# Kernel optimization log

Hardware: AMD Instinct MI355X
Metric: run time of the kernel (lower is better)

Reference implementation:

```python
import jax, jax.numpy as jnp
import numpy as np

NUM_HEADS = 16

def setup_inputs() -> dict:
    key = jax.random.key(0)
    ks = jax.random.split(key, 5)
    B, N, C = 2, 2048, 1024
    x = jax.random.normal(ks[0], (B, N, C), dtype=jnp.float32)
    s_in = 1.0 / np.sqrt(C)
    Wq = jax.random.normal(ks[1], (C, 2 * C), dtype=jnp.float32) * s_in
    Wk = jax.random.normal(ks[2], (C, 2 * C), dtype=jnp.float32) * s_in
    Wv = jax.random.normal(ks[3], (C, 2 * C), dtype=jnp.float32) * s_in
    Wo = jax.random.normal(ks[4], (2 * C, C), dtype=jnp.float32) * (1.0 / np.sqrt(2 * C))
    return {"x": x, "Wq": Wq, "Wk": Wk, "Wv": Wv, "Wo": Wo}

def reference(x, Wq, Wk, Wv, Wo):
    B, N, C = x.shape
    H = NUM_HEADS
    hd = C // H  # head_dim
    def proj(W):
        # [B,N,2C] -> [B,H,N,2*hd]
        return (x @ W).reshape(B, N, H, 2 * hd).transpose(0, 2, 1, 3)
    q = proj(Wq)
    k = proj(Wk)
    v = proj(Wv)
    q_r, q_i = q[..., :hd], q[..., hd:]
    k_r, k_i = k[..., :hd], k[..., hd:]
    v_r, v_i = v[..., :hd], v[..., hd:]
    # complex inner product real part: Re(Q K^H) = q_r.k_r + q_i.k_i
    scores = (jnp.einsum('bhnd,bhmd->bhnm', q_r, k_r)
              + jnp.einsum('bhnd,bhmd->bhnm', q_i, k_i)) / jnp.sqrt(jnp.float32(hd))
    causal = jnp.tril(jnp.ones((N, N), dtype=bool))  # [N,N]
    scores = jnp.where(causal[None, None], scores, -jnp.inf)
    probs = jax.nn.softmax(scores, axis=-1)  # dropout off (eval mode)
    out_r = jnp.einsum('bhnm,bhmd->bhnd', probs, v_r)
    out_i = jnp.einsum('bhnm,bhmd->bhnd', probs, v_i)
    out = jnp.concatenate([out_r, out_i], axis=-1)  # [B,H,N,2*hd]
    out = out.transpose(0, 2, 1, 3).reshape(B, N, 2 * C)
    return out @ Wo  # [B,N,C]
```

## Files before the change

### kernel.cpp

```cpp
#include <hip/hip_runtime.h>
#include <hip/hip_bf16.h>
#include <stdint.h>
#include <cmath>

using bf16 = __hip_bfloat16;
typedef __attribute__((ext_vector_type(8))) short bf16x8;
typedef __attribute__((ext_vector_type(4))) short bf16x4;
typedef __attribute__((ext_vector_type(4))) float f32x4;

#define MFMA16(a, b, c) __builtin_amdgcn_mfma_f32_16x16x32_bf16(a, b, c, 0, 0, 0)

#if defined(__has_builtin)
#if __has_builtin(__builtin_amdgcn_mfma_f32_16x16x16bf16_1k)
#define HAVE_MFMA_K16 1
#endif
#if __has_builtin(__builtin_amdgcn_exp2f)
#define EXP2F __builtin_amdgcn_exp2f
#endif
#endif
#ifndef HAVE_MFMA_K16
#define HAVE_MFMA_K16 0
#endif
#ifndef EXP2F
#define EXP2F exp2f
#endif

#define NEG_BIG (-1e30f)
#define K2SCALE 0.18033688011112042f

__device__ __forceinline__ short f2bf(float v) {
  return __builtin_bit_cast(short, __float2bfloat16(v));
}

__device__ __forceinline__ f32x4 pv_mfma(bf16x4 va, bf16x4 pb, f32x4 c) {
#if HAVE_MFMA_K16
  return __builtin_amdgcn_mfma_f32_16x16x16bf16_1k(va, pb, c, 0, 0, 0);
#else
  const bf16x8 a = {va[0], va[1], va[2], va[3], 0, 0, 0, 0};
  const bf16x8 b = {pb[0], pb[1], pb[2], pb[3], 0, 0, 0, 0};
  return MFMA16(a, b, c);
#endif
}

__device__ __forceinline__ void async_ld16(const bf16* g, bf16* l) {
  __builtin_amdgcn_global_load_lds(
      (const __attribute__((address_space(1))) unsigned int*)g,
      (__attribute__((address_space(3))) unsigned int*)l, 16, 0, 0);
}

template <typename T> __device__ __forceinline__ T cvt_out(float v);
template <> __device__ __forceinline__ float cvt_out<float>(float v) { return v; }
template <> __device__ __forceinline__ bf16 cvt_out<bf16>(float v) { return __float2bfloat16(v); }

__global__ void prep(const float* __restrict__ x,
                     const float* __restrict__ Wq, const float* __restrict__ Wk,
                     const float* __restrict__ Wv, const float* __restrict__ Wo,
                     bf16* __restrict__ xb, bf16* __restrict__ tq,
                     bf16* __restrict__ tk, bf16* __restrict__ tv,
                     bf16* __restrict__ to_) {
  __shared__ bf16 tile[32][33];
  const int bid = blockIdx.x;
  if (bid < 8192) {
    const int z = bid >> 11, tt = bid & 2047;
    const float* in = z == 0 ? Wq : z == 1 ? Wk : z == 2 ? Wv : Wo;
    bf16* out = z == 0 ? tq : z == 1 ? tk : z == 2 ? tv : to_;
    int R, Cc, c0, r0;
    if (z < 3) { R = 1024; Cc = 2048; c0 = (tt & 63) * 32; r0 = (tt >> 6) * 32; }
    else       { R = 2048; Cc = 1024; c0 = (tt & 31) * 32; r0 = (tt >> 5) * 32; }
    const int xx = threadIdx.x & 31;
    const int y = threadIdx.x >> 5;
#pragma unroll
    for (int yy = y; yy < 32; yy += 8)
      tile[yy][xx] = __float2bfloat16(in[(size_t)(r0 + yy) * Cc + c0 + xx]);
    __syncthreads();
#pragma unroll
    for (int yy = y; yy < 32; yy += 8)
      out[(size_t)(c0 + yy) * R + r0 + xx] = tile[xx][yy];
  } else {
    const int i = (bid - 8192) * 256 + threadIdx.x;
    const float4 v = ((const float4*)x)[i];
    bf16 o[4] = {__float2bfloat16(v.x), __float2bfloat16(v.y),
                 __float2bfloat16(v.z), __float2bfloat16(v.w)};
    *(uint64_t*)&xb[i * 4] = *(const uint64_t*)o;
  }
}

__global__ __launch_bounds__(256)
void gemm_qkv(const bf16* __restrict__ xb, const bf16* __restrict__ wq,
              const bf16* __restrict__ wk, const bf16* __restrict__ wv,
              bf16* __restrict__ qo, bf16* __restrict__ ko, bf16* __restrict__ vo) {
  __shared__ __align__(16) bf16 As[128 * 32];
  __shared__ __align__(16) bf16 Bs[128 * 32];
  const int op = blockIdx.y;
  const int bid = blockIdx.x;
  const bf16 *A, *B;
  int m0, n0;
  if (op < 2) { A = xb; B = op ? wk : wq; m0 = (bid >> 4) * 128; n0 = (bid & 15) * 128; }
  else        { A = wv; B = xb;           m0 = (bid & 15) * 128; n0 = (bid >> 4) * 128; }
  const int K = 1024;

  const int t = threadIdx.x;
  const int l = t & 63, w = t >> 6;
  const int q4 = l >> 4, li = l & 15;
  const int wr = (w >> 1) * 64, wc = (w & 1) * 64;

  f32x4 acc[4][4] = {};
  const int colst = (t & 3) * 8;
  const bf16* gA = A + (size_t)m0 * K;
  const bf16* gB = B + (size_t)n0 * K;

  for (int k0 = 0; k0 < K; k0 += 32) {
#pragma unroll
    for (int p = 0; p < 2; ++p) {
      const int row = p * 64 + (t >> 2);
      const int lbase = p * 2048 + (t & ~63) * 8;
      async_ld16(gA + (size_t)row * K + k0 + colst, &As[lbase]);
      async_ld16(gB + (size_t)row * K + k0 + colst, &Bs[lbase]);
    }
    __syncthreads();
    bf16x8 af[4], bfr[4];
#pragma unroll
    for (int i = 0; i < 4; ++i)
      af[i] = *(const bf16x8*)&As[(wr + i * 16 + li) * 32 + q4 * 8];
#pragma unroll
    for (int j = 0; j < 4; ++j)
      bfr[j] = *(const bf16x8*)&Bs[(wc + j * 16 + li) * 32 + q4 * 8];
#pragma unroll
    for (int i = 0; i < 4; ++i)
#pragma unroll
      for (int j = 0; j < 4; ++j)
        acc[i][j] = MFMA16(af[i], bfr[j], acc[i][j]);
    __syncthreads();
  }

#pragma unroll
  for (int i = 0; i < 4; ++i)
#pragma unroll
    for (int j = 0; j < 4; ++j)
#pragma unroll
      for (int r = 0; r < 4; ++r) {
        const int gm = m0 + wr + i * 16 + q4 * 4 + r;
        const int gn = n0 + wc + j * 16 + li;
        const bf16 v = __float2bfloat16(acc[i][j][r]);
        if (op < 2) {
          const int b = gm >> 11, nn = gm & 2047;
          const int h = gn >> 7, d = gn & 127;
          (op ? ko : qo)[((size_t)(b * 16 + h) * 2048 + nn) * 128 + d] = v;
        } else {
          const int h = gm >> 7, d = gm & 127;
          const int b = gn >> 11, nn = gn & 2047;
          vo[((size_t)(b * 16 + h) * 128 + d) * 2048 + nn] = v;
        }
      }
}

template <int NT, typename OT>
__global__ __launch_bounds__(256)
void gemm_bt(const bf16* __restrict__ A, const bf16* __restrict__ B,
             OT* __restrict__ C, int M, int N, int K) {
  __shared__ __align__(16) bf16 As[128 * 32];
  __shared__ __align__(16) bf16 Bs[NT * 32];
  constexpr int JN = NT / 32;
  const int t = threadIdx.x;
  const int l = t & 63, w = t >> 6;
  const int q4 = l >> 4, li = l & 15;
  const int m0 = blockIdx.y * 128;
  const int n0 = blockIdx.x * NT;
  const int wr = (w >> 1) * 64, wc = (w & 1) * (NT / 2);

  f32x4 acc[4][JN] = {};
  const int colst = (t & 3) * 8;
  const bf16* gA = A + (size_t)m0 * K;
  const bf16* gB = B + (size_t)n0 * K;

  for (int k0 = 0; k0 < K; k0 += 32) {
#pragma unroll
    for (int p = 0; p < 2; ++p) {
      const int row = p * 64 + (t >> 2);
      const int lbase = p * 2048 + (t & ~63) * 8;
      async_ld16(gA + (size_t)row * K + k0 + colst, &As[lbase]);
    }
#pragma unroll
    for (int p = 0; p < NT / 64; ++p) {
      const int row = p * 64 + (t >> 2);
      const int lbase = p * 2048 + (t & ~63) * 8;
      async_ld16(gB + (size_t)row * K + k0 + colst, &Bs[lbase]);
    }
    __syncthreads();
    bf16x8 af[4], bfr[JN];
#pragma unroll
    for (int i = 0; i < 4; ++i)
      af[i] = *(const bf16x8*)&As[(wr + i * 16 + li) * 32 + q4 * 8];
#pragma unroll
    for (int j = 0; j < JN; ++j)
      bfr[j] = *(const bf16x8*)&Bs[(wc + j * 16 + li) * 32 + q4 * 8];
#pragma unroll
    for (int i = 0; i < 4; ++i)
#pragma unroll
      for (int j = 0; j < JN; ++j)
        acc[i][j] = MFMA16(af[i], bfr[j], acc[i][j]);
    __syncthreads();
  }

#pragma unroll
  for (int i = 0; i < 4; ++i)
#pragma unroll
    for (int j = 0; j < JN; ++j)
#pragma unroll
      for (int r = 0; r < 4; ++r) {
        const int gm = m0 + wr + i * 16 + q4 * 4 + r;
        const int gn = n0 + wc + j * 16 + li;
        C[(size_t)gm * N + gn] = cvt_out<OT>(acc[i][j][r]);
      }
}

__global__ __launch_bounds__(256, 2)
void flash_attn(const bf16* __restrict__ qm, const bf16* __restrict__ km,
                const bf16* __restrict__ vtm, bf16* __restrict__ om) {
  __shared__ __align__(16) bf16 Ks[2][64 * 128];
  __shared__ __align__(16) bf16 Vts[2][128 * 64];

  const int t = threadIdx.x;
  const int l = t & 63, w = t >> 6;
  const int q4 = l >> 4, li = l & 15;
  const int bh = blockIdx.x;
  const int y = blockIdx.y;
  const int qt = (y < 8) ? 15 - y : y - 8;
  const int qs = qt * 128;
  const size_t qkbase = (size_t)bh * 2048 * 128;
  const size_t vbase = (size_t)bh * 128 * 2048;
  const int b = bh >> 4, h = bh & 15;

  bf16x8 qf[2][4];
#pragma unroll
  for (int g = 0; g < 2; ++g) {
    const bf16* Qb = qm + qkbase + (size_t)(qs + w * 32 + g * 16 + li) * 128;
#pragma unroll
    for (int f = 0; f < 4; ++f)
      qf[g][f] = *(const bf16x8*)(Qb + f * 32 + q4 * 8);
  }

  f32x4 O[2][8] = {};
  float mrun[2] = {NEG_BIG, NEG_BIG}, lrun[2] = {0.f, 0.f};
  const int gmq[2] = {qs + w * 32 + li, qs + w * 32 + 16 + li};

  const int ksrow = t >> 4;
  const int kchu = t & 15;
  const int vsrow = t >> 3;
  const int vchu = t & 7;
  const int wavebase = (t & ~63) * 8;

  const int nt = 2 * qt + 2;

  {
#pragma unroll
    for (int p = 0; p < 4; ++p) {
      const int kr = p * 16 + ksrow;
      async_ld16(km + qkbase + (size_t)kr * 128 + (size_t)((kchu ^ (kr & 7)) * 8),
                 &Ks[0][p * 2048 + wavebase]);
      const int vr = p * 32 + vsrow;
      async_ld16(vtm + vbase + (size_t)vr * 2048 + (size_t)((vchu ^ (vr & 7)) * 8),
                 &Vts[0][p * 2048 + wavebase]);
    }
  }
  asm volatile("s_waitcnt vmcnt(0)" ::: "memory");
  __builtin_amdgcn_s_barrier();
  asm volatile("" ::: "memory");

  int cur = 0;
  for (int j = 0; j < nt; ++j, cur ^= 1) {
    if (j + 1 < nt) {
      const int kn = (j + 1) * 64;
      bf16* kd = &Ks[cur ^ 1][0];
      bf16* vd = &Vts[cur ^ 1][0];
#pragma unroll
      for (int p = 0; p < 4; ++p) {
        const int kr = p * 16 + ksrow;
        async_ld16(km + qkbase + (size_t)(kn + kr) * 128 + (size_t)((kchu ^ (kr & 7)) * 8),
                   kd + p * 2048 + wavebase);
        const int vr = p * 32 + vsrow;
        async_ld16(vtm + vbase + (size_t)vr * 2048 + kn + (size_t)((vchu ^ (vr & 7)) * 8),
                   vd + p * 2048 + wavebase);
      }
    }

    const int kb = j * 64;
    if (!((qs + w * 32 + 31) < kb)) {
      const bool msk = (j >= 2 * qt);
      const bf16* Kc = &Ks[cur][0];
      const bf16* Vc = &Vts[cur][0];

      f32x4 S[2][4];
#pragma unroll
      for (int jk = 0; jk < 4; ++jk) {
        const int krow = jk * 16 + li;
        bf16x8 kf[4];
#pragma unroll
        for (int f = 0; f < 4; ++f)
          kf[f] = *(const bf16x8*)&Kc[krow * 128 + (((f * 4 + q4) ^ (li & 7)) * 8)];
#pragma unroll
        for (int g = 0; g < 2; ++g) {
          f32x4 s = {0.f, 0.f, 0.f, 0.f};
#pragma unroll
          for (int f = 0; f < 4; ++f) s = MFMA16(kf[f], qf[g][f], s);
          S[g][jk] = s;
        }
      }

      bf16x4 pb[2][4];
      float mold[2], nmv[2], rsv[2];
      bool nomove = true;
#pragma unroll
      for (int g = 0; g < 2; ++g) {
        if (msk) {
#pragma unroll
          for (int jk = 0; jk < 4; ++jk)
#pragma unroll
            for (int r = 0; r < 4; ++r)
              if ((kb + jk * 16 + q4 * 4 + r) > gmq[g]) S[g][jk][r] = NEG_BIG;
        }
        float mx = NEG_BIG;
#pragma unroll
        for (int jk = 0; jk < 4; ++jk)
          mx = fmaxf(mx, fmaxf(fmaxf(S[g][jk][0], S[g][jk][1]),
                               fmaxf(S[g][jk][2], S[g][jk][3])));
        mx = fmaxf(mx, __shfl_xor(mx, 16));
        mx = fmaxf(mx, __shfl_xor(mx, 32));
        mold[g] = mrun[g];
        const float nm = fmaxf(mrun[g], mx);
        nomove = nomove && (mx <= mold[g]);
        mrun[g] = nm;
        nmv[g] = nm;
        const float nmk = nm * K2SCALE;
        float rs = 0.f;
#pragma unroll
        for (int jk = 0; jk < 4; ++jk)
#pragma unroll
          for (int r = 0; r < 4; ++r) {
            const float e = EXP2F(__builtin_fmaf(S[g][jk][r], K2SCALE, -nmk));
            rs += e;
            pb[g][jk][r] = f2bf(e);
          }
        rs += __shfl_xor(rs, 16);
        rs += __shfl_xor(rs, 32);
        rsv[g] = rs;
      }

      if (__all(nomove)) {
        lrun[0] += rsv[0];
        lrun[1] += rsv[1];
      } else {
#pragma unroll
        for (int g = 0; g < 2; ++g) {
          const float alpha = EXP2F((mold[g] - nmv[g]) * K2SCALE);
          lrun[g] = lrun[g] * alpha + rsv[g];
#pragma unroll
          for (int dt = 0; dt < 8; ++dt) O[g][dt] *= alpha;
        }
      }

#pragma unroll
      for (int dt = 0; dt < 8; ++dt)
#pragma unroll
        for (int kc = 0; kc < 4; ++kc) {
          const int gc = kc * 2 + (q4 >> 1);
          const bf16x4 va = *(const bf16x4*)&Vc[(dt * 16 + li) * 64 +
                                                ((gc ^ (li & 7)) * 8) +
                                                (q4 & 1) * 4];
          O[0][dt] = pv_mfma(va, pb[0][kc], O[0][dt]);
          O[1][dt] = pv_mfma(va, pb[1][kc], O[1][dt]);
        }
    }

    asm volatile("s_waitcnt vmcnt(0) lgkmcnt(0)" ::: "memory");
    __builtin_amdgcn_s_barrier();
    asm volatile("" ::: "memory");
  }

#pragma unroll
  for (int g = 0; g < 2; ++g) {
    const float inv = 1.0f / lrun[g];
    const size_t orow = (size_t)(b * 2048 + qs + w * 32 + g * 16 + li) * 2048 + h * 128;
#pragma unroll
    for (int dt = 0; dt < 8; ++dt) {
      bf16x4 o4;
#pragma unroll
      for (int r = 0; r < 4; ++r) o4[r] = f2bf(O[g][dt][r] * inv);
      *(bf16x4*)&om[orow + dt * 16 + q4 * 4] = o4;
    }
  }
}

extern "C" void kernel_launch(void* const* d_in, const int* in_sizes, int n_in,
                              void* d_out, int out_size, void* d_ws, size_t ws_size,
                              hipStream_t stream) {
  const float* x = (const float*)d_in[0];
  const float* Wq = (const float*)d_in[1];
  const float* Wk = (const float*)d_in[2];
  const float* Wv = (const float*)d_in[3];
  const float* Wo = (const float*)d_in[4];
  float* out = (float*)d_out;

  bf16* ws = (bf16*)d_ws;
  const size_t MEG = 1u << 20;
  bf16* xb = ws;
  bf16* wTq = ws + 4 * MEG;
  bf16* wTk = ws + 6 * MEG;
  bf16* wTv = ws + 8 * MEG;
  bf16* woT = ws + 10 * MEG;
  bf16* at_ws = ws + 2 * MEG;
  bf16* q_ws = ws + 12 * MEG;
  bf16* k_ws = ws + 20 * MEG;
  bf16* vt_ws = ws + 28 * MEG;

  const dim3 blk(256);

  prep<<<dim3(12288), blk, 0, stream>>>(x, Wq, Wk, Wv, Wo, xb, wTq, wTk, wTv, woT);
  gemm_qkv<<<dim3(512, 3), blk, 0, stream>>>(xb, wTq, wTk, wTv, q_ws, k_ws, vt_ws);
  flash_attn<<<dim3(32, 16), blk, 0, stream>>>(q_ws, k_ws, vt_ws, at_ws);
  gemm_bt<64, float><<<dim3(16, 32), blk, 0, stream>>>(at_ws, woT, out, 4096, 1024, 2048);
}
```

Measured before the change: 280.7 us.

## Shrink flash-attention query tile to 64 rows and read V directly from global

The attention kernel now processes 64 query rows per block (16 per wave) instead of 128, which doubles the grid and raises the launch-bounds occupancy target from 2 to 4 blocks per CU. V tiles are no longer staged in LDS. Each wave reads its V fragments straight from global memory, which halves shared memory use and drops the V async copies. The aim is better occupancy and load balance, at the cost of uncoalesced, unshared global V reads and more redundant K loads across blocks.

```diff
diff --git a/kernel.cpp b/kernel.cpp
--- a/kernel.cpp
+++ b/kernel.cpp
@@ -214,54 +214,47 @@
       }
 }
 
-__global__ __launch_bounds__(256, 2)
+__global__ __launch_bounds__(256, 4)
 void flash_attn(const bf16* __restrict__ qm, const bf16* __restrict__ km,
                 const bf16* __restrict__ vtm, bf16* __restrict__ om) {
   __shared__ __align__(16) bf16 Ks[2][64 * 128];
-  __shared__ __align__(16) bf16 Vts[2][128 * 64];
 
   const int t = threadIdx.x;
   const int l = t & 63, w = t >> 6;
   const int q4 = l >> 4, li = l & 15;
   const int bh = blockIdx.x;
   const int y = blockIdx.y;
-  const int qt = (y < 8) ? 15 - y : y - 8;
-  const int qs = qt * 128;
+  const int qt = (y < 16) ? 31 - y : y - 16;
+  const int qs = qt * 64;
   const size_t qkbase = (size_t)bh * 2048 * 128;
   const size_t vbase = (size_t)bh * 128 * 2048;
   const int b = bh >> 4, h = bh & 15;
 
-  bf16x8 qf[2][4];
-#pragma unroll
-  for (int g = 0; g < 2; ++g) {
-    const bf16* Qb = qm + qkbase + (size_t)(qs + w * 32 + g * 16 + li) * 128;
+  bf16x8 qf[4];
+  {
+    const bf16* Qb = qm + qkbase + (size_t)(qs + w * 16 + li) * 128;
 #pragma unroll
     for (int f = 0; f < 4; ++f)
-      qf[g][f] = *(const bf16x8*)(Qb + f * 32 + q4 * 8);
-  }
-
-  f32x4 O[2][8] = {};
-  float mrun[2] = {NEG_BIG, NEG_BIG}, lrun[2] = {0.f, 0.f};
-  const int gmq[2] = {qs + w * 32 + li, qs + w * 32 + 16 + li};
+      qf[f] = *(const bf16x8*)(Qb + f * 32 + q4 * 8);
+  }
+
+  f32x4 O[8] = {};
+  float mrun = NEG_BIG, lrun = 0.f;
+  const int gmq = qs + w * 16 + li;
 
   const int ksrow = t >> 4;
   const int kchu = t & 15;
-  const int vsrow = t >> 3;
-  const int vchu = t & 7;
   const int wavebase = (t & ~63) * 8;
 
-  const int nt = 2 * qt + 2;
-
-  {
-#pragma unroll
-    for (int p = 0; p < 4; ++p) {
-      const int kr = p * 16 + ksrow;
-      async_ld16(km + qkbase + (size_t)kr * 128 + (size_t)((kchu ^ (kr & 7)) * 8),
-                 &Ks[0][p * 2048 + wavebase]);
-      const int vr = p * 32 + vsrow;
-      async_ld16(vtm + vbase + (size_t)vr * 2048 + (size_t)((vchu ^ (vr & 7)) * 8),
-                 &Vts[0][p * 2048 + wavebase]);
-    }
+  const bf16* vp = vtm + vbase + (size_t)li * 2048 + q4 * 4;
+
+  const int nt = qt + 1;
+
+#pragma unroll
+  for (int p = 0; p < 4; ++p) {
+    const int kr = p * 16 + ksrow;
+    async_ld16(km + qkbase + (size_t)kr * 128 + (size_t)((kchu ^ (kr & 7)) * 8),
+               &Ks[0][p * 2048 + wavebase]);
   }
   asm volatile("s_waitcnt vmcnt(0)" ::: "memory");
   __builtin_amdgcn_s_barrier();
@@ -272,104 +265,84 @@
     if (j + 1 < nt) {
       const int kn = (j + 1) * 64;
       bf16* kd = &Ks[cur ^ 1][0];
-      bf16* vd = &Vts[cur ^ 1][0];
 #pragma unroll
       for (int p = 0; p < 4; ++p) {
         const int kr = p * 16 + ksrow;
         async_ld16(km + qkbase + (size_t)(kn + kr) * 128 + (size_t)((kchu ^ (kr & 7)) * 8),
                    kd + p * 2048 + wavebase);
-        const int vr = p * 32 + vsrow;
-        async_ld16(vtm + vbase + (size_t)vr * 2048 + kn + (size_t)((vchu ^ (vr & 7)) * 8),
-                   vd + p * 2048 + wavebase);
       }
     }
 
     const int kb = j * 64;
-    if (!((qs + w * 32 + 31) < kb)) {
-      const bool msk = (j >= 2 * qt);
-      const bf16* Kc = &Ks[cur][0];
-      const bf16* Vc = &Vts[cur][0];
-
-      f32x4 S[2][4];
-#pragma unroll
-      for (int jk = 0; jk < 4; ++jk) {
-        const int krow = jk * 16 + li;
-        bf16x8 kf[4];
-#pragma unroll
-        for (int f = 0; f < 4; ++f)
-          kf[f] = *(const bf16x8*)&Kc[krow * 128 + (((f * 4 + q4) ^ (li & 7)) * 8)];
-#pragma unroll
-        for (int g = 0; g < 2; ++g) {
-          f32x4 s = {0.f, 0.f, 0.f, 0.f};
-#pragma unroll
-          for (int f = 0; f < 4; ++f) s = MFMA16(kf[f], qf[g][f], s);
-          S[g][jk] = s;
-        }
-      }
-
-      bf16x4 pb[2][4];
-      float mold[2], nmv[2], rsv[2];
-      bool nomove = true;
-#pragma unroll
-      for (int g = 0; g < 2; ++g) {
-        if (msk) {
-#pragma unroll
-          for (int jk = 0; jk < 4; ++jk)
-#pragma unroll
-            for (int r = 0; r < 4; ++r)
-              if ((kb + jk * 16 + q4 * 4 + r) > gmq[g]) S[g][jk][r] = NEG_BIG;
-        }
-        float mx = NEG_BIG;
-#pragma unroll
-        for (int jk = 0; jk < 4; ++jk)
-          mx = fmaxf(mx, fmaxf(fmaxf(S[g][jk][0], S[g][jk][1]),
-                               fmaxf(S[g][jk][2], S[g][jk][3])));
-        mx = fmaxf(mx, __shfl_xor(mx, 16));
-        mx = fmaxf(mx, __shfl_xor(mx, 32));
-        mold[g] = mrun[g];
-        const float nm = fmaxf(mrun[g], mx);
-        nomove = nomove && (mx <= mold[g]);
-        mrun[g] = nm;
-        nmv[g] = nm;
-        const float nmk = nm * K2SCALE;
-        float rs = 0.f;
-#pragma unroll
-        for (int jk = 0; jk < 4; ++jk)
-#pragma unroll
-          for (int r = 0; r < 4; ++r) {
-            const float e = EXP2F(__builtin_fmaf(S[g][jk][r], K2SCALE, -nmk));
-            rs += e;
-            pb[g][jk][r] = f2bf(e);
-          }
-        rs += __shfl_xor(rs, 16);
-        rs += __shfl_xor(rs, 32);
-        rsv[g] = rs;
-      }
-
-      if (__all(nomove)) {
-        lrun[0] += rsv[0];
-        lrun[1] += rsv[1];
-      } else {
-#pragma unroll
-        for (int g = 0; g < 2; ++g) {
-          const float alpha = EXP2F((mold[g] - nmv[g]) * K2SCALE);
-          lrun[g] = lrun[g] * alpha + rsv[g];
-#pragma unroll
-          for (int dt = 0; dt < 8; ++dt) O[g][dt] *= alpha;
-        }
-      }
-
-#pragma unroll
-      for (int dt = 0; dt < 8; ++dt)
-#pragma unroll
-        for (int kc = 0; kc < 4; ++kc) {
-          const int gc = kc * 2 + (q4 >> 1);
-          const bf16x4 va = *(const bf16x4*)&Vc[(dt * 16 + li) * 64 +
-                                                ((gc ^ (li & 7)) * 8) +
-                                                (q4 & 1) * 4];
-          O[0][dt] = pv_mfma(va, pb[0][kc], O[0][dt]);
-          O[1][dt] = pv_mfma(va, pb[1][kc], O[1][dt]);
-        }
+    const bool msk = (j == qt);
+    const bf16* Kc = &Ks[cur][0];
+
+    f32x4 S[4];
+#pragma unroll
+    for (int jk = 0; jk < 4; ++jk) {
+      const int krow = jk * 16 + li;
+      bf16x8 kf[4];
+#pragma unroll
+      for (int f = 0; f < 4; ++f)
+        kf[f] = *(const bf16x8*)&Kc[krow * 128 + (((f * 4 + q4) ^ (li & 7)) * 8)];
+      f32x4 s = {0.f, 0.f, 0.f, 0.f};
+#pragma unroll
+      for (int f = 0; f < 4; ++f) s = MFMA16(kf[f], qf[f], s);
+      S[jk] = s;
+    }
+
+    if (msk) {
+#pragma unroll
+      for (int jk = 0; jk < 4; ++jk)
+#pragma unroll
+        for (int r = 0; r < 4; ++r)
+          if ((kb + jk * 16 + q4 * 4 + r) > gmq) S[jk][r] = NEG_BIG;
+    }
+
+    float mx = NEG_BIG;
+#pragma unroll
+    for (int jk = 0; jk < 4; ++jk)
+      mx = fmaxf(mx, fmaxf(fmaxf(S[jk][0], S[jk][1]), fmaxf(S[jk][2], S[jk][3])));
+    mx = fmaxf(mx, __shfl_xor(mx, 16));
+    mx = fmaxf(mx, __shfl_xor(mx, 32));
+    const float mold = mrun;
+    const float nm = fmaxf(mrun, mx);
+    const bool nomove = (mx <= mold);
+    mrun = nm;
+    const float nmk = nm * K2SCALE;
+
+    bf16x4 pb[4];
+    float rs = 0.f;
+#pragma unroll
+    for (int jk = 0; jk < 4; ++jk) {
+      float e[4];
+#pragma unroll
+      for (int r = 0; r < 4; ++r) {
+        e[r] = EXP2F(__builtin_fmaf(S[jk][r], K2SCALE, -nmk));
+        pb[jk][r] = f2bf(e[r]);
+      }
+      rs += (e[0] + e[1]) + (e[2] + e[3]);
+    }
+    rs += __shfl_xor(rs, 16);
+    rs += __shfl_xor(rs, 32);
+
+    if (__all(nomove)) {
+      lrun += rs;
+    } else {
+      const float alpha = EXP2F((mold - nm) * K2SCALE);
+      lrun = lrun * alpha + rs;
+#pragma unroll
+      for (int dt = 0; dt < 8; ++dt) O[dt] *= alpha;
+    }
+
+#pragma unroll
+    for (int dt = 0; dt < 8; ++dt) {
+      const bf16* vr = vp + (size_t)dt * 16 * 2048 + kb;
+#pragma unroll
+      for (int kc = 0; kc < 4; ++kc) {
+        const bf16x4 va = *(const bf16x4*)(vr + kc * 16);
+        O[dt] = pv_mfma(va, pb[kc], O[dt]);
+      }
     }
 
     asm volatile("s_waitcnt vmcnt(0) lgkmcnt(0)" ::: "memory");
@@ -377,15 +350,14 @@
     asm volatile("" ::: "memory");
   }
 
-#pragma unroll
-  for (int g = 0; g < 2; ++g) {
-    const float inv = 1.0f / lrun[g];
-    const size_t orow = (size_t)(b * 2048 + qs + w * 32 + g * 16 + li) * 2048 + h * 128;
+  {
+    const float inv = 1.0f / lrun;
+    const size_t orow = (size_t)(b * 2048 + qs + w * 16 + li) * 2048 + h * 128;
 #pragma unroll
     for (int dt = 0; dt < 8; ++dt) {
       bf16x4 o4;
 #pragma unroll
-      for (int r = 0; r < 4; ++r) o4[r] = f2bf(O[g][dt][r] * inv);
+      for (int r = 0; r < 4; ++r) o4[r] = f2bf(O[dt][r] * inv);
       *(bf16x4*)&om[orow + dt * 16 + q4 * 4] = o4;
     }
   }
@@ -417,6 +389,6 @@
 
   prep<<<dim3(12288), blk, 0, stream>>>(x, Wq, Wk, Wv, Wo, xb, wTq, wTk, wTv, woT);
   gemm_qkv<<<dim3(512, 3), blk, 0, stream>>>(xb, wTq, wTk, wTv, q_ws, k_ws, vt_ws);
-  flash_attn<<<dim3(32, 16), blk, 0, stream>>>(q_ws, k_ws, vt_ws, at_ws);
+  flash_attn<<<dim3(32, 32), blk, 0, stream>>>(q_ws, k_ws, vt_ws, at_ws);
   gemm_bt<64, float><<<dim3(16, 32), blk, 0, stream>>>(at_ws, woT, out, 4096, 1024, 2048);
 }
```

After: 459.8 us. 63.8% more time.
